# Kernel tuning notes

Measured on AMD Instinct MI355X. Metric: run time of the kernel, lower is better.

## Reference

```python
import jax, jax.numpy as jnp
import numpy as np

N_CELLS = 50000
N_GENES = 2000
B = 1024
K = 16
H = 256
IN_DIM = 2 * N_GENES  # spliced + unspliced concatenated


def setup_inputs() -> dict:
    key = jax.random.key(0)
    ks = jax.random.split(key, 16)
    def u(k, shape):
        return jax.random.uniform(k, shape, dtype=jnp.float32)
    def w_init(k, shape, scale=0.02):
        return jax.random.normal(k, shape, dtype=jnp.float32) * scale
    return {
        "encoder_input": jax.random.normal(ks[0], (B, IN_DIM), dtype=jnp.float32),
        "neighbor_index": jax.random.randint(ks[1], (B, K), 0, N_CELLS),
        "neighbor_weight": u(ks[2], (B, K)),
        "neighbor_index2": jax.random.randint(ks[3], (B, K), 0, N_CELLS),
        "neighbor_weight2": u(ks[4], (B, K)),
        "spliced_full": u(ks[5], (N_CELLS, N_GENES)),
        "unspliced_full": u(ks[6], (N_CELLS, N_GENES)),
        # projection MLP
        "W1": w_init(ks[7], (IN_DIM, H)), "b1": jnp.zeros((H,), jnp.float32),
        "W2": w_init(ks[8], (H, H)), "b2": jnp.zeros((H,), jnp.float32),
        # attention MLP
        "Wa1": w_init(ks[9], (IN_DIM, H)), "ba1": jnp.zeros((H,), jnp.float32),
        "Wa2": w_init(ks[10], (H, 1)), "ba2": jnp.zeros((1,), jnp.float32),
        # difference projection
        "Wd": w_init(ks[11], (IN_DIM, H)), "bd": jnp.zeros((H,), jnp.float32),
        # residual projection
        "Wr": w_init(ks[12], (IN_DIM, H)), "br": jnp.zeros((H,), jnp.float32),
        # layer norm + gates (gates init to zero like nn.Parameter(torch.zeros(...)))
        "ln_gamma": jnp.ones((H,), jnp.float32), "ln_beta": jnp.zeros((H,), jnp.float32),
        "message_gate": jnp.zeros((H,), jnp.float32),
        "cross_graph_gate": jnp.zeros((H,), jnp.float32),
    }


def reference(encoder_input, neighbor_index, neighbor_weight, neighbor_index2,
              neighbor_weight2, spliced_full, unspliced_full,
              W1, b1, W2, b2, Wa1, ba1, Wa2, ba2, Wd, bd, Wr, br,
              ln_gamma, ln_beta, message_gate, cross_graph_gate):
    # Dropout is inference-mode identity.
    def gather_feats(idx):
        # idx: [B,K] -> [B,K,2G], log1p-style transform (log_variational=True)
        sp = jnp.log(0.01 + spliced_full[idx])
        un = jnp.log(0.01 + unspliced_full[idx])
        return jnp.concatenate([sp, un], axis=-1)

    def attend_normalize(nf, w):
        # attention MLP: Linear -> Tanh -> Linear(1), softmax over K
        att = jnp.tanh(nf @ Wa1 + ba1) @ Wa2 + ba2  # [B,K,1]
        att = jax.nn.softmax(att[..., 0], axis=1)   # [B,K]
        w = w * att
        return w / (jnp.sum(w, axis=1, keepdims=True) + 1e-12)

    def project(x):
        h = jax.nn.relu(x @ W1 + b1)
        return jax.nn.relu(h @ W2 + b2)

    nf = gather_feats(neighbor_index)                      # [B,K,2G]
    w = attend_normalize(nf, neighbor_weight)              # [B,K]
    projected = project(jnp.einsum('bk,bkd->bd', w, nf))   # [B,H]

    nf2 = gather_feats(neighbor_index2)
    w2 = attend_normalize(nf2, neighbor_weight2)
    proj2 = project(jnp.einsum('bk,bkd->bd', w2, nf2))
    g = jax.nn.sigmoid(cross_graph_gate)
    projected = g * projected + (1.0 - g) * proj2

    # use_differences
    diff_sum = jnp.einsum('bk,bkd->bd', w, nf - encoder_input[:, None, :])
    projected = projected + jax.nn.relu(diff_sum @ Wd + bd)

    # use_residual
    projected = projected + jax.nn.relu(encoder_input @ Wr + br)

    # use_gate: LayerNorm then sigmoid-gated scale
    mu = jnp.mean(projected, axis=-1, keepdims=True)
    var = jnp.var(projected, axis=-1, keepdims=True)
    projected = (projected - mu) * jax.lax.rsqrt(var + 1e-5) * ln_gamma + ln_beta
    projected = jax.nn.sigmoid(message_gate) * projected

    return jnp.concatenate([encoder_input, projected], axis=-1)  # [B, 2G+H]
```

## Files before the change

kernel.cpp:

```cpp
#include <hip/hip_runtime.h>
#include <cstdint>
#include <cstddef>

typedef short v8s __attribute__((ext_vector_type(8)));
typedef float v4f __attribute__((ext_vector_type(4)));

#define NG   2000
#define IND  4000
#define HDIM 256
#define OUTW 4256

__device__ __forceinline__ unsigned short f2bf(float f) {
  unsigned a = __builtin_bit_cast(unsigned, f);
  a += 0x7fffu + ((a >> 16) & 1u);
  return (unsigned short)(a >> 16);
}
__device__ __forceinline__ unsigned pk2bf(float lo, float hi) {
  unsigned a = __builtin_bit_cast(unsigned, lo);
  unsigned b = __builtin_bit_cast(unsigned, hi);
  a += 0x7fffu + ((a >> 16) & 1u);
  b += 0x7fffu + ((b >> 16) & 1u);
  return (a >> 16) | (b & 0xffff0000u);
}
__device__ __forceinline__ void async16(const void* g, void* l) {
  __builtin_amdgcn_global_load_lds(
      (const __attribute__((address_space(1))) unsigned int*)g,
      (__attribute__((address_space(3))) unsigned int*)l, 16, 0, 0);
}

__global__ void k_transpose(const float* __restrict__ w1, const float* __restrict__ wa1,
                            const float* __restrict__ wd, const float* __restrict__ wr,
                            unsigned short* __restrict__ ws0) {
  __shared__ float tl[32][33];
  int mat = blockIdx.z;
  const float* src = (mat == 0) ? wa1 : (mat == 1) ? w1 : (mat == 2) ? wd : wr;
  unsigned short* dst = ws0 + (size_t)mat * 1024000;
  int j0 = blockIdx.x * 32, c0 = blockIdx.y * 32;
  int tx = threadIdx.x, ty = threadIdx.y;
  for (int jj = ty; jj < 32; jj += 8)
    tl[jj][tx] = src[(size_t)(j0 + jj) * HDIM + c0 + tx];
  __syncthreads();
  for (int cc = ty; cc < 32; cc += 8)
    dst[(size_t)(c0 + cc) * IND + j0 + tx] = f2bf(tl[tx][cc]);
}

__global__ void k_enc_copy(const float* __restrict__ enc, float* __restrict__ out,
                           unsigned short* __restrict__ eb) {
  int c = blockIdx.x * 256 + threadIdx.x;
  int b = blockIdx.y;
  if (c < IND) {
    float v = enc[(size_t)b * IND + c];
    out[(size_t)b * OUTW + c] = v;
    eb[(size_t)b * IND + c] = f2bf(v);
  }
}

__global__ void __launch_bounds__(256) k_logits(
    const int* __restrict__ nidx1, const int* __restrict__ nidx2,
    const float* __restrict__ sp, const float* __restrict__ un,
    const unsigned short* __restrict__ Wa1T,
    const float* __restrict__ ba1, const float* __restrict__ Wa2,
    const float* __restrict__ ba2, float* __restrict__ logits) {
  __shared__ __align__(16) unsigned short a_tile[256 * 32];
  __shared__ __align__(16) unsigned short b_tile[64 * 32];
  __shared__ int scell[64];
  __shared__ float red[4][64];

  const int t = threadIdx.x;
  const int wave = t >> 6, lane = t & 63;
  const int row_base = blockIdx.x * 64;

  if (t < 64) {
    int r = row_base + t;
    scell[t] = (r < 16384) ? nidx1[r] : nidx2[r - 16384];
  }
  __syncthreads();

  const int lrow = lane & 15, kgrp = lane >> 4;
  const int brow = t >> 2, bpart = t & 3;
  const size_t cellbase = (size_t)scell[brow] * NG;

  v4f acc[4][4];
#pragma unroll
  for (int i = 0; i < 4; i++)
#pragma unroll
    for (int j = 0; j < 4; j++) acc[i][j] = (v4f)0.f;

  for (int kt = 0; kt < 125; ++kt) {
#pragma unroll
    for (int j = 0; j < 4; ++j) {
      int c = (wave * 4 + j) * 64 + lane;
      int wcol = c >> 2, part = c & 3;
      async16(Wa1T + (size_t)wcol * IND + kt * 32 + part * 8,
              (char*)a_tile + (size_t)c * 16);
    }
    {
      int col0 = kt * 32 + bpart * 8;
      const float* src = (col0 < NG) ? (sp + cellbase + col0) : (un + cellbase + (col0 - NG));
      float4 v0 = reinterpret_cast<const float4*>(src)[0];
      float4 v1 = reinterpret_cast<const float4*>(src)[1];
      uint4 pk;
      pk.x = pk2bf(__logf(0.01f + v0.x), __logf(0.01f + v0.y));
      pk.y = pk2bf(__logf(0.01f + v0.z), __logf(0.01f + v0.w));
      pk.z = pk2bf(__logf(0.01f + v1.x), __logf(0.01f + v1.y));
      pk.w = pk2bf(__logf(0.01f + v1.z), __logf(0.01f + v1.w));
      reinterpret_cast<uint4*>(b_tile)[t] = pk;
    }
    __syncthreads();
    v8s bf[4];
#pragma unroll
    for (int nt = 0; nt < 4; nt++)
      bf[nt] = *reinterpret_cast<const v8s*>(&b_tile[(nt * 16 + lrow) * 32 + kgrp * 8]);
#pragma unroll
    for (int mt = 0; mt < 4; mt++) {
      v8s af = *reinterpret_cast<const v8s*>(&a_tile[(wave * 64 + mt * 16 + lrow) * 32 + kgrp * 8]);
#pragma unroll
      for (int nt = 0; nt < 4; nt++)
        acc[mt][nt] = __builtin_amdgcn_mfma_f32_16x16x32_bf16(af, bf[nt], acc[mt][nt], 0, 0, 0);
    }
    __syncthreads();
  }

  float partial[4] = {0.f, 0.f, 0.f, 0.f};
#pragma unroll
  for (int mt = 0; mt < 4; mt++) {
#pragma unroll
    for (int r = 0; r < 4; r++) {
      int wcol = wave * 64 + mt * 16 + kgrp * 4 + r;
      float bb = ba1[wcol], wv = Wa2[wcol];
#pragma unroll
      for (int nt = 0; nt < 4; nt++) {
        float h = acc[mt][nt][r] + bb;
        float th = 1.f - 2.f / (1.f + __expf(2.f * h));
        partial[nt] += th * wv;
      }
    }
  }
#pragma unroll
  for (int nt = 0; nt < 4; nt++) {
    float p = partial[nt];
    p += __shfl_xor(p, 16);
    p += __shfl_xor(p, 32);
    if (lane < 16) red[wave][nt * 16 + lane] = p;
  }
  __syncthreads();
  if (t < 64)
    logits[row_base + t] = red[0][t] + red[1][t] + red[2][t] + red[3][t] + ba2[0];
}

__global__ void k_softmax(const float* __restrict__ logits,
                          const float* __restrict__ nw1, const float* __restrict__ nw2,
                          float* __restrict__ wnorm, float* __restrict__ wsum) {
  int t = threadIdx.x;
  int gb = blockIdx.x * 16 + (t >> 4);
  int k = t & 15;
  float lg = logits[gb * 16 + k];
  float mx = lg;
#pragma unroll
  for (int m = 1; m < 16; m <<= 1) mx = fmaxf(mx, __shfl_xor(mx, m));
  float e = __expf(lg - mx);
  float s = e;
#pragma unroll
  for (int m = 1; m < 16; m <<= 1) s += __shfl_xor(s, m);
  float att = e / s;
  float nw = (gb < 1024) ? nw1[gb * 16 + k] : nw2[(gb - 1024) * 16 + k];
  float w = nw * att;
  float S = w;
#pragma unroll
  for (int m = 1; m < 16; m <<= 1) S += __shfl_xor(S, m);
  wnorm[gb * 16 + k] = w / (S + 1e-12f);
  if (k == 0) wsum[gb] = S / (S + 1e-12f);
}

__global__ void __launch_bounds__(256) k_wsum(
    const int* __restrict__ nidx1, const int* __restrict__ nidx2,
    const float* __restrict__ sp, const float* __restrict__ un,
    const float* __restrict__ enc,
    const float* __restrict__ wnorm, const float* __restrict__ wsum,
    unsigned short* __restrict__ xb, unsigned short* __restrict__ db) {
  __shared__ size_t cb[16];
  __shared__ float wv[16];
  int gb = blockIdx.x, t = threadIdx.x;
  int g = gb >> 10, b = gb & 1023;
  if (t < 16) {
    int cell = (g == 0 ? nidx1 : nidx2)[b * 16 + t];
    cb[t] = (size_t)cell * NG;
    wv[t] = wnorm[gb * 16 + t];
  }
  __syncthreads();
  float ws = wsum[gb];
  for (int i = 0; i < 16; ++i) {
    int c = i * 256 + t;
    if (c >= IND) continue;
    const float* basep = (c < NG) ? sp : un;
    int cc = (c < NG) ? c : c - NG;
    float acc = 0.f;
#pragma unroll
    for (int k = 0; k < 16; ++k)
      acc += wv[k] * __logf(0.01f + basep[cb[k] + cc]);
    xb[(size_t)gb * IND + c] = f2bf(acc);
    if (g == 0) {
      float d = acc - ws * enc[(size_t)b * IND + c];
      db[(size_t)b * IND + c] = f2bf(d);
    }
  }
}

__global__ void __launch_bounds__(256) k_gemm256(
    const unsigned short* __restrict__ xb, const unsigned short* __restrict__ dbA,
    const unsigned short* __restrict__ ebA,
    const unsigned short* __restrict__ W1T, const unsigned short* __restrict__ WdT,
    const unsigned short* __restrict__ WrT,
    const float* __restrict__ b1, const float* __restrict__ bd, const float* __restrict__ br,
    float* __restrict__ h1, float* __restrict__ dout, float* __restrict__ rout) {
  __shared__ __align__(16) unsigned short a_tile[256 * 32];
  __shared__ __align__(16) unsigned short b_tile[64 * 32];
  int bz = blockIdx.x;
  const unsigned short *A, *WT;
  const float* bias;
  float* out;
  int rowbase;
  if (bz < 32)      { A = xb;  WT = W1T; bias = b1; out = h1;   rowbase = bz * 64; }
  else if (bz < 48) { A = dbA; WT = WdT; bias = bd; out = dout; rowbase = (bz - 32) * 64; }
  else              { A = ebA; WT = WrT; bias = br; out = rout; rowbase = (bz - 48) * 64; }

  const int t = threadIdx.x, wave = t >> 6, lane = t & 63;
  const int lrow = lane & 15, kgrp = lane >> 4;
  v4f acc[4][4];
#pragma unroll
  for (int i = 0; i < 4; i++)
#pragma unroll
    for (int j = 0; j < 4; j++) acc[i][j] = (v4f)0.f;

  for (int kt = 0; kt < 125; ++kt) {
#pragma unroll
    for (int j = 0; j < 4; ++j) {
      int c = (wave * 4 + j) * 64 + lane;
      int wcol = c >> 2, part = c & 3;
      async16(WT + (size_t)wcol * IND + kt * 32 + part * 8,
              (char*)a_tile + (size_t)c * 16);
    }
    {
      int c = wave * 64 + lane;
      int row = c >> 2, part = c & 3;
      async16(A + (size_t)(rowbase + row) * IND + kt * 32 + part * 8,
              (char*)b_tile + (size_t)c * 16);
    }
    __syncthreads();
    v8s bf[4];
#pragma unroll
    for (int nt = 0; nt < 4; nt++)
      bf[nt] = *reinterpret_cast<const v8s*>(&b_tile[(nt * 16 + lrow) * 32 + kgrp * 8]);
#pragma unroll
    for (int mt = 0; mt < 4; mt++) {
      v8s af = *reinterpret_cast<const v8s*>(&a_tile[(wave * 64 + mt * 16 + lrow) * 32 + kgrp * 8]);
#pragma unroll
      for (int nt = 0; nt < 4; nt++)
        acc[mt][nt] = __builtin_amdgcn_mfma_f32_16x16x32_bf16(af, bf[nt], acc[mt][nt], 0, 0, 0);
    }
    __syncthreads();
  }
#pragma unroll
  for (int mt = 0; mt < 4; mt++) {
#pragma unroll
    for (int r = 0; r < 4; r++) {
      int ocol = wave * 64 + mt * 16 + kgrp * 4 + r;
      float bs = bias[ocol];
#pragma unroll
      for (int nt = 0; nt < 4; nt++) {
        int row = nt * 16 + lrow;
        out[(size_t)(rowbase + row) * HDIM + ocol] = fmaxf(acc[mt][nt][r] + bs, 0.f);
      }
    }
  }
}

__global__ void __launch_bounds__(256) k_final(
    const float* __restrict__ h1, const float* __restrict__ dbuf, const float* __restrict__ rbuf,
    const float* __restrict__ W2, const float* __restrict__ b2,
    const float* __restrict__ mgate, const float* __restrict__ cgate,
    const float* __restrict__ gamma, const float* __restrict__ beta,
    float* __restrict__ out) {
  __shared__ float ha[256], hb[256];
  __shared__ float redbuf[8];
  int b = blockIdx.x, t = threadIdx.x;
  ha[t] = h1[b * 256 + t];
  hb[t] = h1[(1024 + b) * 256 + t];
  __syncthreads();
  float s1 = 0.f, s2 = 0.f;
#pragma unroll 8
  for (int j = 0; j < 256; ++j) {
    float w = W2[j * 256 + t];
    s1 = fmaf(ha[j], w, s1);
    s2 = fmaf(hb[j], w, s2);
  }
  float bb = b2[t];
  float h2a = fmaxf(s1 + bb, 0.f), h2b = fmaxf(s2 + bb, 0.f);
  float g = 1.f / (1.f + __expf(-cgate[t]));
  float p = g * h2a + (1.f - g) * h2b + dbuf[b * 256 + t] + rbuf[b * 256 + t];
  float sum = p, sumsq = p * p;
#pragma unroll
  for (int m = 1; m < 64; m <<= 1) {
    sum += __shfl_xor(sum, m);
    sumsq += __shfl_xor(sumsq, m);
  }
  int wave = t >> 6, lane = t & 63;
  if (lane == 0) { redbuf[wave] = sum; redbuf[4 + wave] = sumsq; }
  __syncthreads();
  sum = redbuf[0] + redbuf[1] + redbuf[2] + redbuf[3];
  sumsq = redbuf[4] + redbuf[5] + redbuf[6] + redbuf[7];
  float mu = sum * (1.f / 256.f);
  float var = sumsq * (1.f / 256.f) - mu * mu;
  float rs = rsqrtf(var + 1e-5f);
  float y = (p - mu) * rs * gamma[t] + beta[t];
  y *= 1.f / (1.f + __expf(-mgate[t]));
  out[(size_t)b * OUTW + 4000 + t] = y;
}

extern "C" void kernel_launch(void* const* d_in, const int* in_sizes, int n_in,
                              void* d_out, int out_size, void* d_ws, size_t ws_size,
                              hipStream_t stream) {
  const float* enc  = (const float*)d_in[0];
  const int* ni1    = (const int*)d_in[1];
  const float* nw1  = (const float*)d_in[2];
  const int* ni2    = (const int*)d_in[3];
  const float* nw2  = (const float*)d_in[4];
  const float* sp   = (const float*)d_in[5];
  const float* un   = (const float*)d_in[6];
  const float* W1   = (const float*)d_in[7];
  const float* b1   = (const float*)d_in[8];
  const float* W2   = (const float*)d_in[9];
  const float* b2   = (const float*)d_in[10];
  const float* Wa1  = (const float*)d_in[11];
  const float* ba1  = (const float*)d_in[12];
  const float* Wa2  = (const float*)d_in[13];
  const float* ba2  = (const float*)d_in[14];
  const float* Wd   = (const float*)d_in[15];
  const float* bd   = (const float*)d_in[16];
  const float* Wr   = (const float*)d_in[17];
  const float* br   = (const float*)d_in[18];
  const float* gam  = (const float*)d_in[19];
  const float* bet  = (const float*)d_in[20];
  const float* mg   = (const float*)d_in[21];
  const float* cg   = (const float*)d_in[22];

  char* ws = (char*)d_ws;
  unsigned short* Wa1T = (unsigned short*)(ws + 0);
  unsigned short* W1T  = (unsigned short*)(ws + 2048000);
  unsigned short* WdT  = (unsigned short*)(ws + 4096000);
  unsigned short* WrT  = (unsigned short*)(ws + 6144000);
  unsigned short* XB   = (unsigned short*)(ws + 8192000);
  unsigned short* DB   = (unsigned short*)(ws + 24576000);
  unsigned short* EB   = (unsigned short*)(ws + 32768000);
  float* H1   = (float*)(ws + 40960000);
  float* DBUF = (float*)(ws + 43057152);
  float* RBUF = (float*)(ws + 44105728);
  float* LOG  = (float*)(ws + 45154304);
  float* WN   = (float*)(ws + 45285376);
  float* WSUM = (float*)(ws + 45416448);

  float* out = (float*)d_out;

  hipLaunchKernelGGL(k_transpose, dim3(125, 8, 4), dim3(32, 8), 0, stream,
                     W1, Wa1, Wd, Wr, (unsigned short*)ws);
  hipLaunchKernelGGL(k_enc_copy, dim3(16, 1024), dim3(256), 0, stream, enc, out, EB);
  hipLaunchKernelGGL(k_logits, dim3(512), dim3(256), 0, stream,
                     ni1, ni2, sp, un, Wa1T, ba1, Wa2, ba2, LOG);
  hipLaunchKernelGGL(k_softmax, dim3(128), dim3(256), 0, stream, LOG, nw1, nw2, WN, WSUM);
  hipLaunchKernelGGL(k_wsum, dim3(2048), dim3(256), 0, stream,
                     ni1, ni2, sp, un, enc, WN, WSUM, XB, DB);
  hipLaunchKernelGGL(k_gemm256, dim3(64), dim3(256), 0, stream,
                     XB, DB, EB, W1T, WdT, WrT, b1, bd, br, H1, DBUF, RBUF);
  hipLaunchKernelGGL(k_final, dim3(1024), dim3(256), 0, stream,
                     H1, DBUF, RBUF, W2, b2, mg, cg, gam, bet, out);
}
```

Before: 1.171 ms.

## Split-K the 256-wide GEMMs, fuse softmax into wsum, prefetch gathers in logits

The 64-block GEMM kernel becomes a 4-way split-K launch with 256 blocks. It writes partial sums to a workspace, and the final kernel reduces them and applies bias and ReLU, which raises occupancy on a GPU with many CUs. The separate softmax kernel is folded into the weighted-sum kernel, so one launch and an intermediate buffer round trip go away. In the logits kernel, the next tile's gathered spliced/unspliced values are register-prefetched while the current tile is converted, and one barrier is dropped. The cost is extra partial-sum traffic through global memory.

```diff
diff --git a/kernel.cpp b/kernel.cpp
--- a/kernel.cpp
+++ b/kernel.cpp
@@ -86,7 +86,29 @@
 #pragma unroll
     for (int j = 0; j < 4; j++) acc[i][j] = (v4f)0.f;
 
+  float4 c0, c1;
+  {
+    int col0 = bpart * 8;
+    const float* src = sp + cellbase + col0;
+    c0 = reinterpret_cast<const float4*>(src)[0];
+    c1 = reinterpret_cast<const float4*>(src)[1];
+  }
+
   for (int kt = 0; kt < 125; ++kt) {
+    uint4 pk;
+    pk.x = pk2bf(__logf(0.01f + c0.x), __logf(0.01f + c0.y));
+    pk.y = pk2bf(__logf(0.01f + c0.z), __logf(0.01f + c0.w));
+    pk.z = pk2bf(__logf(0.01f + c1.x), __logf(0.01f + c1.y));
+    pk.w = pk2bf(__logf(0.01f + c1.z), __logf(0.01f + c1.w));
+    __syncthreads();
+    float4 n0, n1;
+    if (kt < 124) {
+      int col0 = (kt + 1) * 32 + bpart * 8;
+      const float* src = (col0 < NG) ? (sp + cellbase + col0) : (un + cellbase + (col0 - NG));
+      n0 = reinterpret_cast<const float4*>(src)[0];
+      n1 = reinterpret_cast<const float4*>(src)[1];
+    }
+    reinterpret_cast<uint4*>(b_tile)[t] = pk;
 #pragma unroll
     for (int j = 0; j < 4; ++j) {
       int c = (wave * 4 + j) * 64 + lane;
@@ -94,18 +116,6 @@
       async16(Wa1T + (size_t)wcol * IND + kt * 32 + part * 8,
               (char*)a_tile + (size_t)c * 16);
     }
-    {
-      int col0 = kt * 32 + bpart * 8;
-      const float* src = (col0 < NG) ? (sp + cellbase + col0) : (un + cellbase + (col0 - NG));
-      float4 v0 = reinterpret_cast<const float4*>(src)[0];
-      float4 v1 = reinterpret_cast<const float4*>(src)[1];
-      uint4 pk;
-      pk.x = pk2bf(__logf(0.01f + v0.x), __logf(0.01f + v0.y));
-      pk.y = pk2bf(__logf(0.01f + v0.z), __logf(0.01f + v0.w));
-      pk.z = pk2bf(__logf(0.01f + v1.x), __logf(0.01f + v1.y));
-      pk.w = pk2bf(__logf(0.01f + v1.z), __logf(0.01f + v1.w));
-      reinterpret_cast<uint4*>(b_tile)[t] = pk;
-    }
     __syncthreads();
     v8s bf[4];
 #pragma unroll
@@ -118,7 +128,7 @@
       for (int nt = 0; nt < 4; nt++)
         acc[mt][nt] = __builtin_amdgcn_mfma_f32_16x16x32_bf16(af, bf[nt], acc[mt][nt], 0, 0, 0);
     }
-    __syncthreads();
+    if (kt < 124) { c0 = n0; c1 = n1; }
   }
 
   float partial[4] = {0.f, 0.f, 0.f, 0.f};
@@ -148,47 +158,40 @@
     logits[row_base + t] = red[0][t] + red[1][t] + red[2][t] + red[3][t] + ba2[0];
 }
 
-__global__ void k_softmax(const float* __restrict__ logits,
-                          const float* __restrict__ nw1, const float* __restrict__ nw2,
-                          float* __restrict__ wnorm, float* __restrict__ wsum) {
-  int t = threadIdx.x;
-  int gb = blockIdx.x * 16 + (t >> 4);
-  int k = t & 15;
-  float lg = logits[gb * 16 + k];
-  float mx = lg;
-#pragma unroll
-  for (int m = 1; m < 16; m <<= 1) mx = fmaxf(mx, __shfl_xor(mx, m));
-  float e = __expf(lg - mx);
-  float s = e;
-#pragma unroll
-  for (int m = 1; m < 16; m <<= 1) s += __shfl_xor(s, m);
-  float att = e / s;
-  float nw = (gb < 1024) ? nw1[gb * 16 + k] : nw2[(gb - 1024) * 16 + k];
-  float w = nw * att;
-  float S = w;
-#pragma unroll
-  for (int m = 1; m < 16; m <<= 1) S += __shfl_xor(S, m);
-  wnorm[gb * 16 + k] = w / (S + 1e-12f);
-  if (k == 0) wsum[gb] = S / (S + 1e-12f);
-}
-
 __global__ void __launch_bounds__(256) k_wsum(
     const int* __restrict__ nidx1, const int* __restrict__ nidx2,
     const float* __restrict__ sp, const float* __restrict__ un,
     const float* __restrict__ enc,
-    const float* __restrict__ wnorm, const float* __restrict__ wsum,
+    const float* __restrict__ logits,
+    const float* __restrict__ nw1, const float* __restrict__ nw2,
     unsigned short* __restrict__ xb, unsigned short* __restrict__ db) {
   __shared__ size_t cb[16];
   __shared__ float wv[16];
+  __shared__ float wsum_s;
   int gb = blockIdx.x, t = threadIdx.x;
   int g = gb >> 10, b = gb & 1023;
   if (t < 16) {
     int cell = (g == 0 ? nidx1 : nidx2)[b * 16 + t];
     cb[t] = (size_t)cell * NG;
-    wv[t] = wnorm[gb * 16 + t];
-  }
-  __syncthreads();
-  float ws = wsum[gb];
+    float lg = logits[gb * 16 + t];
+    float mx = lg;
+#pragma unroll
+    for (int m = 1; m < 16; m <<= 1) mx = fmaxf(mx, __shfl_xor(mx, m));
+    float e = __expf(lg - mx);
+    float s = e;
+#pragma unroll
+    for (int m = 1; m < 16; m <<= 1) s += __shfl_xor(s, m);
+    float att = e / s;
+    float nw = (g == 0) ? nw1[b * 16 + t] : nw2[b * 16 + t];
+    float w = nw * att;
+    float S = w;
+#pragma unroll
+    for (int m = 1; m < 16; m <<= 1) S += __shfl_xor(S, m);
+    wv[t] = w / (S + 1e-12f);
+    if (t == 0) wsum_s = S / (S + 1e-12f);
+  }
+  __syncthreads();
+  float ws = wsum_s;
   for (int i = 0; i < 16; ++i) {
     int c = i * 256 + t;
     if (c >= IND) continue;
@@ -211,18 +214,19 @@
     const unsigned short* __restrict__ ebA,
     const unsigned short* __restrict__ W1T, const unsigned short* __restrict__ WdT,
     const unsigned short* __restrict__ WrT,
-    const float* __restrict__ b1, const float* __restrict__ bd, const float* __restrict__ br,
-    float* __restrict__ h1, float* __restrict__ dout, float* __restrict__ rout) {
+    float* __restrict__ P) {
   __shared__ __align__(16) unsigned short a_tile[256 * 32];
   __shared__ __align__(16) unsigned short b_tile[64 * 32];
   int bz = blockIdx.x;
+  int chunk = bz >> 6, tile = bz & 63;
+  const int kstart[5] = {0, 32, 63, 94, 125};
+  int k0 = kstart[chunk], k1 = kstart[chunk + 1];
+
   const unsigned short *A, *WT;
-  const float* bias;
-  float* out;
-  int rowbase;
-  if (bz < 32)      { A = xb;  WT = W1T; bias = b1; out = h1;   rowbase = bz * 64; }
-  else if (bz < 48) { A = dbA; WT = WdT; bias = bd; out = dout; rowbase = (bz - 32) * 64; }
-  else              { A = ebA; WT = WrT; bias = br; out = rout; rowbase = (bz - 48) * 64; }
+  int rowbase, growbase;
+  if (tile < 32)      { A = xb;  WT = W1T; rowbase = tile * 64;        growbase = rowbase; }
+  else if (tile < 48) { A = dbA; WT = WdT; rowbase = (tile - 32) * 64; growbase = 2048 + rowbase; }
+  else                { A = ebA; WT = WrT; rowbase = (tile - 48) * 64; growbase = 3072 + rowbase; }
 
   const int t = threadIdx.x, wave = t >> 6, lane = t & 63;
   const int lrow = lane & 15, kgrp = lane >> 4;
@@ -232,7 +236,7 @@
 #pragma unroll
     for (int j = 0; j < 4; j++) acc[i][j] = (v4f)0.f;
 
-  for (int kt = 0; kt < 125; ++kt) {
+  for (int kt = k0; kt < k1; ++kt) {
 #pragma unroll
     for (int j = 0; j < 4; ++j) {
       int c = (wave * 4 + j) * 64 + lane;
@@ -265,18 +269,18 @@
 #pragma unroll
     for (int r = 0; r < 4; r++) {
       int ocol = wave * 64 + mt * 16 + kgrp * 4 + r;
-      float bs = bias[ocol];
 #pragma unroll
       for (int nt = 0; nt < 4; nt++) {
         int row = nt * 16 + lrow;
-        out[(size_t)(rowbase + row) * HDIM + ocol] = fmaxf(acc[mt][nt][r] + bs, 0.f);
+        P[((size_t)chunk * 4096 + growbase + row) * HDIM + ocol] = acc[mt][nt][r];
       }
     }
   }
 }
 
 __global__ void __launch_bounds__(256) k_final(
-    const float* __restrict__ h1, const float* __restrict__ dbuf, const float* __restrict__ rbuf,
+    const float* __restrict__ P,
+    const float* __restrict__ b1, const float* __restrict__ bd, const float* __restrict__ br,
     const float* __restrict__ W2, const float* __restrict__ b2,
     const float* __restrict__ mgate, const float* __restrict__ cgate,
     const float* __restrict__ gamma, const float* __restrict__ beta,
@@ -284,8 +288,19 @@
   __shared__ float ha[256], hb[256];
   __shared__ float redbuf[8];
   int b = blockIdx.x, t = threadIdx.x;
-  ha[t] = h1[b * 256 + t];
-  hb[t] = h1[(1024 + b) * 256 + t];
+  float sa = 0.f, sb = 0.f, sd = 0.f, sr = 0.f;
+#pragma unroll
+  for (int c = 0; c < 4; ++c) {
+    const float* base = P + (size_t)c * 4096 * HDIM;
+    sa += base[(size_t)b * HDIM + t];
+    sb += base[(size_t)(1024 + b) * HDIM + t];
+    sd += base[(size_t)(2048 + b) * HDIM + t];
+    sr += base[(size_t)(3072 + b) * HDIM + t];
+  }
+  ha[t] = fmaxf(sa + b1[t], 0.f);
+  hb[t] = fmaxf(sb + b1[t], 0.f);
+  float dv = fmaxf(sd + bd[t], 0.f);
+  float rv = fmaxf(sr + br[t], 0.f);
   __syncthreads();
   float s1 = 0.f, s2 = 0.f;
 #pragma unroll 8
@@ -297,7 +312,7 @@
   float bb = b2[t];
   float h2a = fmaxf(s1 + bb, 0.f), h2b = fmaxf(s2 + bb, 0.f);
   float g = 1.f / (1.f + __expf(-cgate[t]));
-  float p = g * h2a + (1.f - g) * h2b + dbuf[b * 256 + t] + rbuf[b * 256 + t];
+  float p = g * h2a + (1.f - g) * h2b + dv + rv;
   float sum = p, sumsq = p * p;
 #pragma unroll
   for (int m = 1; m < 64; m <<= 1) {
@@ -352,12 +367,8 @@
   unsigned short* XB   = (unsigned short*)(ws + 8192000);
   unsigned short* DB   = (unsigned short*)(ws + 24576000);
   unsigned short* EB   = (unsigned short*)(ws + 32768000);
-  float* H1   = (float*)(ws + 40960000);
-  float* DBUF = (float*)(ws + 43057152);
-  float* RBUF = (float*)(ws + 44105728);
-  float* LOG  = (float*)(ws + 45154304);
-  float* WN   = (float*)(ws + 45285376);
-  float* WSUM = (float*)(ws + 45416448);
+  float* P    = (float*)(ws + 40960000);
+  float* LOG  = (float*)(ws + 57737216);
 
   float* out = (float*)d_out;
 
@@ -366,11 +377,10 @@
   hipLaunchKernelGGL(k_enc_copy, dim3(16, 1024), dim3(256), 0, stream, enc, out, EB);
   hipLaunchKernelGGL(k_logits, dim3(512), dim3(256), 0, stream,
                      ni1, ni2, sp, un, Wa1T, ba1, Wa2, ba2, LOG);
-  hipLaunchKernelGGL(k_softmax, dim3(128), dim3(256), 0, stream, LOG, nw1, nw2, WN, WSUM);
   hipLaunchKernelGGL(k_wsum, dim3(2048), dim3(256), 0, stream,
-                     ni1, ni2, sp, un, enc, WN, WSUM, XB, DB);
-  hipLaunchKernelGGL(k_gemm256, dim3(64), dim3(256), 0, stream,
-                     XB, DB, EB, W1T, WdT, WrT, b1, bd, br, H1, DBUF, RBUF);
+                     ni1, ni2, sp, un, enc, LOG, nw1, nw2, XB, DB);
+  hipLaunchKernelGGL(k_gemm256, dim3(256), dim3(256), 0, stream,
+                     XB, DB, EB, W1T, WdT, WrT, P);
   hipLaunchKernelGGL(k_final, dim3(1024), dim3(256), 0, stream,
-                     H1, DBUF, RBUF, W2, b2, mg, cg, gam, bet, out);
-}
+                     P, b1, bd, br, W2, b2, mg, cg, gam, bet, out);
+}
```

Result: faster. 1.045 ms (-10.8%).
